# Performance work log

Hardware: AMD Instinct MI355X
Metric: run time of the kernel (lower is better)

Reference implementation:

```python
import jax, jax.numpy as jnp
import numpy as np

NEG = -9.0e15


def setup_inputs() -> dict:
    key = jax.random.key(0)
    k_x, k_w, k_e, k_b, k_m = jax.random.split(key, 5)
    B, N, C, F = 2048, 64, 256, 256
    x = jax.random.normal(k_x, (B, N, C), dtype=jnp.float32)
    W = jax.random.normal(k_w, (2, C, F), dtype=jnp.float32) * (1.414 / np.sqrt(C + F))
    # full logit tensor; only entries where mask holds are ever read (equivalent
    # to torch's flat `e` scattered into the nonzero positions of adj)
    e = jax.random.normal(k_e, (F, N, N), dtype=jnp.float32)
    bias = jax.random.normal(k_b, (F,), dtype=jnp.float32) * (1.0 / np.sqrt(C))
    # symmetric adjacency mask with self-loops, density ~0.3
    m = jax.random.bernoulli(k_m, 0.3, (N, N))
    mask = (m | m.T) | jnp.eye(N, dtype=bool)
    return {"x": x, "W": W, "e": e, "bias": bias, "mask": mask}


def reference(x, W, e, bias, mask):
    # x: [B,N,C], W: [2,C,F], e: [F,N,N], bias: [F], mask: [N,N] bool
    h0 = x @ W[0]                                   # [B,N,F] (self term)
    h1 = x @ W[1]                                   # [B,N,F] (neighbor term)
    logits = jnp.where(mask[None, :, :], e, NEG)    # [F,N,N]
    adj = jax.nn.softmax(logits, axis=2)            # per-channel row softmax
    N = mask.shape[0]
    eye = jnp.eye(N, dtype=bool)
    d = jnp.diagonal(adj, axis1=1, axis2=2)         # [F,N]  (adj * E diagonal)
    off = jnp.where(eye[None, :, :], 0.0, adj)      # [F,N,N] (adj * (1-E))
    # (adj*E) @ h0 reduces to per-node diagonal scaling; off-diag is a
    # per-channel NxN matmul batched over B.
    out = d.T[None, :, :] * h0 + jnp.einsum('fnm,bmf->bnf', off, h1)
    return out + bias[None, None, :]
```

## Files before the change

kernel.cpp:

```cpp
#include <hip/hip_runtime.h>
#include <hip/hip_bf16.h>


typedef __attribute__((ext_vector_type(8))) short  fragA;
typedef __attribute__((ext_vector_type(4))) float  f32x4;
typedef __attribute__((ext_vector_type(8))) unsigned short u16x8;
typedef __attribute__((ext_vector_type(4))) unsigned short u16x4;

constexpr long OFF_OFF = 0;
constexpr long OFF_WT  = 2l * 1024 * 1024;
constexpr long OFF_DS  = OFF_WT + 512l * 256 * 2;
constexpr long OFF_XB  = OFF_DS + 64l * 256 * 4;
constexpr long OFF_G0  = OFF_XB + 131072l * 256 * 2;
constexpr long OFF_H1T = OFF_G0 + 131072l * 256 * 2;
constexpr long WS_NEED = OFF_H1T + 131072l * 256 * 2;

static __device__ inline unsigned short f2bf(float f) {
  __hip_bfloat16 h = __float2bfloat16(f);
  return __builtin_bit_cast(unsigned short, h);
}
static __device__ inline float bf2f(unsigned short u) {
  unsigned int x = ((unsigned int)u) << 16;
  return __builtin_bit_cast(float, x);
}
static __device__ inline unsigned int packbf(float a, float b) {
  return (unsigned int)f2bf(a) | ((unsigned int)f2bf(b) << 16);
}
static __device__ __forceinline__ void gl16(const void* g, void* l) {
  __builtin_amdgcn_global_load_lds(
      (const __attribute__((address_space(1))) unsigned int*)g,
      (__attribute__((address_space(3))) unsigned int*)l, 16, 0, 0);
}
static __device__ __forceinline__ f32x4 mfma16(fragA a, fragA b, f32x4 c) {
  return __builtin_amdgcn_mfma_f32_16x16x32_bf16(a, b, c, 0, 0, 0);
}

__global__ __launch_bounds__(256) void k_pre(const float* __restrict__ x,
                                             const float* __restrict__ e,
                                             const float* __restrict__ W,
                                             const unsigned char* __restrict__ mask,
                                             char* __restrict__ ws_b) {
  const int bid = blockIdx.x;
  const int tid = threadIdx.x;
  if (bid < 4096) {
    unsigned short* off = (unsigned short*)(ws_b + OFF_OFF);
    float* dscale = (float*)(ws_b + OFF_DS);
    const int lane = tid & 63;
    const int row  = bid * 4 + (tid >> 6);
    const int n = row & 63;
    bool is_u8 = __all(mask[lane * 65] != 0);
    bool mv;
    if (is_u8) mv = mask[n * 64 + lane] != 0;
    else       mv = ((const int*)mask)[n * 64 + lane] != 0;
    float v = mv ? e[(long)row * 64 + lane] : -1e30f;
    float mx = v;
#pragma unroll
    for (int s = 32; s; s >>= 1) mx = fmaxf(mx, __shfl_xor(mx, s));
    float ex = mv ? __expf(v - mx) : 0.f;
    float sm = ex;
#pragma unroll
    for (int s = 32; s; s >>= 1) sm += __shfl_xor(sm, s);
    float adj = ex / sm;
    const int f = row >> 6;
    if (lane == n) dscale[n * 256 + f] = adj;
    off[(long)row * 64 + lane] = f2bf(lane == n ? 0.f : adj);
  } else if (bid < 6144) {
    unsigned short* xb = (unsigned short*)(ws_b + OFF_XB);
    long i = ((long)(bid - 4096) * 256 + tid) * 8;
    const long stride = 2048l * 256 * 8;
    const long total = 131072l * 256;
    for (; i < total; i += stride) {
      float4 a = *(const float4*)(x + i);
      float4 b = *(const float4*)(x + i + 4);
      u16x8 p;
      p[0] = f2bf(a.x); p[1] = f2bf(a.y); p[2] = f2bf(a.z); p[3] = f2bf(a.w);
      p[4] = f2bf(b.x); p[5] = f2bf(b.y); p[6] = f2bf(b.z); p[7] = f2bf(b.w);
      *(u16x8*)(xb + i) = p;
    }
  } else {
    unsigned short* Wt = (unsigned short*)(ws_b + OFF_WT);
    __shared__ float t[64][65];
    const int b2 = bid - 6144;
    const int w = b2 >> 4, f0 = ((b2 >> 2) & 3) * 64, c0 = (b2 & 3) * 64;
    const int tr = tid >> 2, tc = (tid & 3) * 16;
    const float* src = W + ((long)(w * 256 + c0 + tr)) * 256 + f0 + tc;
#pragma unroll
    for (int i = 0; i < 16; i += 4) {
      float4 v = *(const float4*)(src + i);
      t[tr][tc + i] = v.x; t[tr][tc + i + 1] = v.y;
      t[tr][tc + i + 2] = v.z; t[tr][tc + i + 3] = v.w;
    }
    __syncthreads();
    u16x8 p0, p1;
#pragma unroll
    for (int i = 0; i < 8; i++)  p0[i] = f2bf(t[tc + i][tr]);
#pragma unroll
    for (int i = 0; i < 8; i++)  p1[i] = f2bf(t[tc + 8 + i][tr]);
    unsigned short* dst = Wt + ((long)(w * 256 + f0 + tr)) * 256 + c0 + tc;
    *(u16x8*)dst = p0;
    *(u16x8*)(dst + 8) = p1;
  }
}

__global__ __launch_bounds__(256, 5) void k_gemm(char* __restrict__ ws_b) {
  const float* dscale = (const float*)(ws_b + OFF_DS);
  const char* xb_b = ws_b + OFF_XB;
  const char* wt_b = ws_b + OFF_WT;
  unsigned short* g0g = (unsigned short*)(ws_b + OFF_G0);
  unsigned short* h1t = (unsigned short*)(ws_b + OFF_H1T);

  __shared__ __align__(16) char arena[24576];

  const int tid = threadIdx.x;
  const int wid = tid >> 6, lane = tid & 63;
  const int lr = lane & 15, qu = lane >> 4;

  const int wg = blockIdx.x;
  const int xcd = wg & 7, s = wg >> 3;
  const int rg = xcd * 128 + (s >> 3);
  const int cg = s & 7;
  const int f0 = cg * 32;
  const long R0 = (long)rg * 128;

  const int ar   = tid >> 3;
  const int aswz = (((tid & 7) ^ (ar & 7)) << 4);
  const int wrow0 = f0 + ar;
  const int wrow1 = 256 + f0 + ar;

  auto STAGE = [&](int ks) {
    const long ko = (long)ks * 128;
#pragma unroll
    for (int i = 0; i < 4; i++)
      gl16(xb_b + (R0 + i * 32 + ar) * 512 + ko + aswz,
           arena + i * 4096 + tid * 16);
    gl16(wt_b + (long)wrow0 * 512 + ko + aswz, arena + 16384 + tid * 16);
    gl16(wt_b + (long)wrow1 * 512 + ko + aswz, arena + 16384 + 4096 + tid * 16);
  };

  STAGE(0);
  f32x4 acc[2][4] = {};
  const int arow0 = wid * 32;

  for (int ks = 0; ks < 4; ks++) {
    __syncthreads();
#pragma unroll
    for (int kk = 0; kk < 2; kk++) {
      fragA af[2], bfr[4];
#pragma unroll
      for (int i2 = 0; i2 < 2; i2++) {
        int r = arow0 + i2 * 16 + lr;
        af[i2] = *(const fragA*)(arena + r * 128 +
                     ((kk * 64 + qu * 16) ^ ((lr & 7) << 4)));
      }
#pragma unroll
      for (int j = 0; j < 4; j++) {
        int cc = j * 16 + lr;
        bfr[j] = *(const fragA*)(arena + 16384 + cc * 128 +
                     ((kk * 64 + qu * 16) ^ ((lr & 7) << 4)));
      }
#pragma unroll
      for (int i2 = 0; i2 < 2; i2++)
#pragma unroll
        for (int j = 0; j < 4; j++)
          acc[i2][j] = mfma16(af[i2], bfr[j], acc[i2][j]);
    }
    __syncthreads();
    if (ks < 3) STAGE(ks + 1);
  }

  unsigned short* Gs = (unsigned short*)(arena);
  unsigned short* Ts = (unsigned short*)(arena + 10240);
#pragma unroll
  for (int i2 = 0; i2 < 2; i2++) {
#pragma unroll
    for (int j = 0; j < 2; j++) {
      int f = f0 + j * 16 + lr;
#pragma unroll
      for (int r = 0; r < 4; r++) {
        int rloc = arow0 + i2 * 16 + qu * 4 + r;
        int n = rloc & 63;
        Gs[rloc * 40 + j * 16 + lr] = f2bf(dscale[n * 256 + f] * acc[i2][j][r]);
      }
    }
#pragma unroll
    for (int j = 2; j < 4; j++) {
      int fl = (j - 2) * 16 + lr;
      int rb = arow0 + i2 * 16 + qu * 4;
      u16x4 pk;
      pk[0] = f2bf(acc[i2][j][0]); pk[1] = f2bf(acc[i2][j][1]);
      pk[2] = f2bf(acc[i2][j][2]); pk[3] = f2bf(acc[i2][j][3]);
      *(u16x4*)(Ts + fl * 136 + rb) = pk;
    }
  }
  __syncthreads();

  {
    int row = tid >> 1, half = tid & 1;
    const unsigned short* sp = Gs + row * 40 + half * 16;
    unsigned short* dp = g0g + (R0 + row) * 256 + f0 + half * 16;
    *(u16x8*)dp = *(const u16x8*)sp;
    *(u16x8*)(dp + 8) = *(const u16x8*)(sp + 8);
  }
  {
    int f = tid >> 3, seg = tid & 7;
    const unsigned short* sp = Ts + f * 136 + seg * 16;
    unsigned short* dp = h1t + (long)(f0 + f) * 131072 + R0 + seg * 16;
    *(u16x8*)dp = *(const u16x8*)sp;
    *(u16x8*)(dp + 8) = *(const u16x8*)(sp + 8);
  }
}

__global__ __launch_bounds__(256, 5) void k_eout(const float* __restrict__ bias,
                                                 const char* __restrict__ ws_b,
                                                 float* __restrict__ out) {
  const unsigned short* offp = (const unsigned short*)(ws_b + OFF_OFF);
  const unsigned short* h1t  = (const unsigned short*)(ws_b + OFF_H1T);
  const unsigned short* g0g  = (const unsigned short*)(ws_b + OFF_G0);

  const int tid = threadIdx.x;
  const int wid = tid >> 6, lane = tid & 63;
  const int lr = lane & 15, qu = lane >> 4;

  const int wg = blockIdx.x;
  const int xcd = wg & 7, u = wg >> 3;
  const int bg = xcd * 16 + (u >> 4);
  const int fg = u & 15;
  const long B0 = (long)bg * 16;
  const int f0 = fg * 16;
  const int nw = wid * 16;

  const unsigned short* obase = offp + (long)f0 * 4096 + (nw + lr) * 64 + qu * 8;
  const unsigned short* hbase = h1t + (long)f0 * 131072 + (B0 + lr) * 64 + qu * 8;

  unsigned int eb[4][8];

#pragma unroll
  for (int fp = 0; fp < 8; fp++) {
    const unsigned short* ob0 = obase + (long)(2 * fp) * 4096;
    const unsigned short* hb0 = hbase + (long)(2 * fp) * 131072;
    const unsigned short* ob1 = ob0 + 4096;
    const unsigned short* hb1 = hb0 + 131072;
    fragA oa0 = *(const fragA*)(ob0);
    fragA oa1 = *(const fragA*)(ob0 + 32);
    fragA ha0 = *(const fragA*)(hb0);
    fragA ha1 = *(const fragA*)(hb0 + 32);
    fragA oc0 = *(const fragA*)(ob1);
    fragA oc1 = *(const fragA*)(ob1 + 32);
    fragA hc0 = *(const fragA*)(hb1);
    fragA hc1 = *(const fragA*)(hb1 + 32);
    f32x4 e0 = {}, e1 = {};
    e0 = mfma16(oa0, ha0, e0);
    e1 = mfma16(oc0, hc0, e1);
    e0 = mfma16(oa1, ha1, e0);
    e1 = mfma16(oc1, hc1, e1);
#pragma unroll
    for (int j = 0; j < 4; j++)
      eb[j][fp] = packbf(e0[j], e1[j]);
  }

  float4 bv[4];
#pragma unroll
  for (int k = 0; k < 4; k++) bv[k] = ((const float4*)(bias + f0))[k];

#pragma unroll
  for (int j = 0; j < 4; j++) {
    long R = (B0 + lr) * 64 + nw + qu * 4 + j;
    const unsigned short* gp = g0g + R * 256 + f0;
    u16x8 gv0 = ((const u16x8*)gp)[0];
    u16x8 gv1 = ((const u16x8*)gp)[1];
    float4* op = (float4*)(out + R * 256 + f0);
#pragma unroll
    for (int k = 0; k < 4; k++) {
      unsigned int p0 = eb[j][k * 2], p1 = eb[j][k * 2 + 1];
      float g0e = bf2f(k < 2 ? gv0[k * 4 + 0] : gv1[(k - 2) * 4 + 0]);
      float g1e = bf2f(k < 2 ? gv0[k * 4 + 1] : gv1[(k - 2) * 4 + 1]);
      float g2e = bf2f(k < 2 ? gv0[k * 4 + 2] : gv1[(k - 2) * 4 + 2]);
      float g3e = bf2f(k < 2 ? gv0[k * 4 + 3] : gv1[(k - 2) * 4 + 3]);
      float4 ov;
      ov.x = g0e + bf2f((unsigned short)(p0 & 0xffff)) + bv[k].x;
      ov.y = g1e + bf2f((unsigned short)(p0 >> 16)) + bv[k].y;
      ov.z = g2e + bf2f((unsigned short)(p1 & 0xffff)) + bv[k].z;
      ov.w = g3e + bf2f((unsigned short)(p1 >> 16)) + bv[k].w;
      op[k] = ov;
    }
  }
}

extern "C" void kernel_launch(void* const* d_in, const int* in_sizes, int n_in,
                              void* d_out, int out_size, void* d_ws, size_t ws_size,
                              hipStream_t stream) {
  const float* x    = (const float*)d_in[0];
  const float* W    = (const float*)d_in[1];
  const float* e    = (const float*)d_in[2];
  const float* bias = (const float*)d_in[3];
  const unsigned char* mask = (const unsigned char*)d_in[4];
  float* out = (float*)d_out;
  char* ws = (char*)d_ws;
  if (ws_size < (size_t)WS_NEED) return;

  k_pre<<<6176, 256, 0, stream>>>(x, e, W, mask, ws);
  k_gemm<<<8192, 256, 0, stream>>>(ws);
  k_eout<<<2048, 256, 0, stream>>>(bias, ws, out);
}
```

Baseline: 241.6 us.

## Stage h1t and off tiles in swizzled LDS with double-buffered off loads

The output kernel now loads its h1t tile for all 16 channels and the per-channel off matrices into a 48KB shared-memory arena, using XOR-swizzled addresses. The off matrix is double-buffered, with the next channel's load issued while the current channel is consumed. Previously each of the four waves fetched the same fragments separately from global memory, so this is meant to remove redundant global/L2 traffic and share data across waves. The cost is a barrier per channel iteration (16 per block), a larger LDS footprint, and a launch bound lowered from 5 to 4 blocks per CU.

```diff
diff --git a/kernel.cpp b/kernel.cpp
--- a/kernel.cpp
+++ b/kernel.cpp
@@ -210,12 +210,14 @@
   }
 }
 
-__global__ __launch_bounds__(256, 5) void k_eout(const float* __restrict__ bias,
+__global__ __launch_bounds__(256, 4) void k_eout(const float* __restrict__ bias,
                                                  const char* __restrict__ ws_b,
                                                  float* __restrict__ out) {
-  const unsigned short* offp = (const unsigned short*)(ws_b + OFF_OFF);
-  const unsigned short* h1t  = (const unsigned short*)(ws_b + OFF_H1T);
-  const unsigned short* g0g  = (const unsigned short*)(ws_b + OFF_G0);
+  const char* off_b = ws_b + OFF_OFF;
+  const char* h1t_b = ws_b + OFF_H1T;
+  const unsigned short* g0g = (const unsigned short*)(ws_b + OFF_G0);
+
+  __shared__ __align__(16) char arena[49152];
 
   const int tid = threadIdx.x;
   const int wid = tid >> 6, lane = tid & 63;
@@ -229,33 +231,53 @@
   const int f0 = fg * 16;
   const int nw = wid * 16;
 
-  const unsigned short* obase = offp + (long)f0 * 4096 + (nw + lr) * 64 + qu * 8;
-  const unsigned short* hbase = h1t + (long)f0 * 131072 + (B0 + lr) * 64 + qu * 8;
+  {
+    const int bb = (tid & 127) >> 3;
+    const int sw = ((tid & 7) ^ (bb & 7)) << 4;
+#pragma unroll
+    for (int i = 0; i < 8; i++) {
+      int f = f0 + i * 2 + (tid >> 7);
+      gl16(h1t_b + (long)f * 262144 + bg * 2048 + bb * 128 + sw,
+           arena + i * 4096 + tid * 16);
+    }
+  }
+  const int onr = tid >> 3;
+  const int osw = ((tid & 7) ^ (onr & 7)) << 4;
+  {
+#pragma unroll
+    for (int j = 0; j < 2; j++)
+      gl16(off_b + (long)f0 * 8192 + j * 4096 + onr * 128 + osw,
+           arena + 32768 + j * 4096 + tid * 16);
+  }
 
   unsigned int eb[4][8];
-
-#pragma unroll
-  for (int fp = 0; fp < 8; fp++) {
-    const unsigned short* ob0 = obase + (long)(2 * fp) * 4096;
-    const unsigned short* hb0 = hbase + (long)(2 * fp) * 131072;
-    const unsigned short* ob1 = ob0 + 4096;
-    const unsigned short* hb1 = hb0 + 131072;
-    fragA oa0 = *(const fragA*)(ob0);
-    fragA oa1 = *(const fragA*)(ob0 + 32);
-    fragA ha0 = *(const fragA*)(hb0);
-    fragA ha1 = *(const fragA*)(hb0 + 32);
-    fragA oc0 = *(const fragA*)(ob1);
-    fragA oc1 = *(const fragA*)(ob1 + 32);
-    fragA hc0 = *(const fragA*)(hb1);
-    fragA hc1 = *(const fragA*)(hb1 + 32);
-    f32x4 e0 = {}, e1 = {};
-    e0 = mfma16(oa0, ha0, e0);
-    e1 = mfma16(oc0, hc0, e1);
-    e0 = mfma16(oa1, ha1, e0);
-    e1 = mfma16(oc1, hc1, e1);
-#pragma unroll
-    for (int j = 0; j < 4; j++)
-      eb[j][fp] = packbf(e0[j], e1[j]);
+  f32x4 ep;
+
+#pragma unroll
+  for (int fi = 0; fi < 16; fi++) {
+    __syncthreads();
+    if (fi < 15) {
+#pragma unroll
+      for (int j = 0; j < 2; j++)
+        gl16(off_b + (long)(f0 + fi + 1) * 8192 + j * 4096 + onr * 128 + osw,
+             arena + 32768 + ((fi + 1) & 1) * 8192 + j * 4096 + tid * 16);
+    }
+    const char* ob = arena + 32768 + (fi & 1) * 8192;
+    const char* hb = arena + fi * 2048;
+    f32x4 e = {};
+#pragma unroll
+    for (int kk = 0; kk < 2; kk++) {
+      int n = nw + lr;
+      fragA a = *(const fragA*)(ob + n * 128 + (((kk * 4 + qu) ^ (n & 7)) << 4));
+      fragA b = *(const fragA*)(hb + lr * 128 + (((kk * 4 + qu) ^ (lr & 7)) << 4));
+      e = mfma16(a, b, e);
+    }
+    if (fi & 1) {
+#pragma unroll
+      for (int j = 0; j < 4; j++) eb[j][fi >> 1] = packbf(ep[j], e[j]);
+    } else {
+      ep = e;
+    }
   }
 
   float4 bv[4];
```

Result: faster. 208.7 us (-13.6%).
